# Optimization experiments

Hardware: AMD Instinct MI355X
Metric: run time of the kernel (lower is better)

Reference implementation:

```python
import jax, jax.numpy as jnp
import numpy as np

EPS_SIM = 1e-10
EPS_NORM = 1e-12


def setup_inputs() -> dict:
    key = jax.random.key(0)
    k1, k2, k3, k4, k5 = jax.random.split(key, 5)
    B, CH, H, W = 64, 512, 28, 28
    R = CH // 16  # reduction
    x = jax.random.normal(k1, (B, CH, H, W), dtype=jnp.float32)
    # torch nn.Linear weights are [out, in]
    wD = jax.random.normal(k2, (R, CH), dtype=jnp.float32) * (1.0 / np.sqrt(CH))
    bD = jax.random.normal(k3, (R,), dtype=jnp.float32) * 0.01
    wU = jax.random.normal(k4, (CH, R), dtype=jnp.float32) * (1.0 / np.sqrt(R))
    bU = jax.random.normal(k5, (CH,), dtype=jnp.float32) * 0.01
    return {"x": x, "wD": wD, "bD": bD, "wU": wU, "bU": bU}


def _hybrid_weight(xap):
    # xap: [B, CH, N]; returns row-diag-masked, globally normalized similarity Wij [B, CH, CH]
    gram = jnp.einsum('bin,bjn->bij', xap, xap)           # [B,CH,CH]
    sq = jnp.sum(xap * xap, axis=-1)                      # [B,CH]
    d2 = sq[:, :, None] + sq[:, None, :] - 2.0 * gram
    d = jnp.sqrt(d2)
    d = jnp.where(jnp.isnan(d), 0.0, d)                   # NaN mask (sqrt of negatives)
    d = jnp.maximum(d, 0.0)                               # clamp(0, inf)
    mean_d = jnp.mean(d, axis=(1, 2), keepdims=True)
    l2_sim = jnp.exp(-d / (mean_d + EPS_SIM))
    w = jnp.sqrt(sq)                                      # per-channel L2 norm
    denom = jnp.maximum(w[:, :, None] * w[:, None, :], EPS_SIM)
    cos = gram / denom
    cos = jnp.where(jnp.isnan(cos), 0.0, cos)
    cos = jnp.maximum(cos, 0.0)
    sim = cos * l2_sim
    CH = sim.shape[1]
    sim = sim * (1.0 - jnp.eye(CH, dtype=sim.dtype))      # zero diagonal
    Wij = sim / (jnp.sum(sim, axis=(1, 2), keepdims=True) + EPS_SIM)
    return Wij


def reference(x, wD, bD, wU, bU):
    B, CH, H, W = x.shape
    r = 7  # rdim[512]
    # adaptive avg pool to 7x7 (H, W divisible by 7 -> exact block average)
    xap = x.reshape(B, CH, r, H // r, r, W // r).mean(axis=(3, 5)).reshape(B, CH, r * r)
    Wij = jax.lax.stop_gradient(_hybrid_weight(xap))      # computed under no_grad in torch
    gap = x.mean(axis=(2, 3))                             # [B,CH] global avg pool
    mu = gap.mean(axis=1, keepdims=True)
    std = jnp.std(gap, axis=1, ddof=1, keepdims=True)     # torch std is unbiased
    z = (gap - mu) / std                                  # [B,CH]
    # diag(z z^T Wij)_i = z_i * (z^T Wij)_i  -> avoid materializing zz^T
    local_mi = z * jnp.einsum('bj,bji->bi', z, Wij)       # [B,CH]
    m = local_mi.mean(axis=1, keepdims=True)
    s = jnp.std(local_mi, axis=1, ddof=1, keepdims=True)
    ch = (local_mi - m) / (s + EPS_NORM)                  # normal_G
    h = jax.nn.relu(ch @ wD.T + bD)
    att = h @ wU.T + bU
    scale = jax.nn.sigmoid(att)[:, :, None, None]
    return x * scale
```

## Files before the change

kernel.cpp:

```cpp
#include <hip/hip_runtime.h>
#include <hip/hip_bf16.h>
#include <stdint.h>

#define NB 64
#define NC 512
#define NHW 784
#define NK 49
#define KP 64
#define NR 32

typedef short sh8 __attribute__((ext_vector_type(8)));
typedef float f32x4 __attribute__((ext_vector_type(4)));
typedef int v4i __attribute__((ext_vector_type(4)));

__device__ __forceinline__ float wave_sum(float v) {
#pragma unroll
  for (int o = 32; o; o >>= 1) v += __shfl_xor(v, o);
  return v;
}

__global__ __launch_bounds__(256) void pool_kernel(const float* __restrict__ x,
                                                   __hip_bfloat16* __restrict__ xap,
                                                   float* __restrict__ wbuf,
                                                   float* __restrict__ gap) {
  int wid = threadIdx.x >> 6, lane = threadIdx.x & 63;
  int row = blockIdx.x * 4 + wid;
  const float* xr = x + (size_t)row * NHW;
  float bin = 0.f;
  if (lane < NK) {
    int pr = lane / 7, pc = lane - pr * 7;
    const float4* p = (const float4*)(xr + pr * 112 + pc * 4);
    float s = 0.f;
#pragma unroll
    for (int i = 0; i < 4; ++i) {
      float4 v = p[i * 7];
      s += (v.x + v.y) + (v.z + v.w);
    }
    bin = s * 0.0625f;
  }
  float s1 = wave_sum(bin);
  float s2 = wave_sum(bin * bin);
  xap[(size_t)row * KP + lane] = __float2bfloat16(bin);
  if (lane == 0) {
    wbuf[row] = sqrtf(s2);
    gap[row] = s1 * (1.f / 49.f);
  }
}

__global__ __launch_bounds__(256) void zstat_kernel(const float* __restrict__ gap,
                                                    float* __restrict__ z) {
  __shared__ float red[4];
  int b = blockIdx.x, t = threadIdx.x;
  int wid = t >> 6, lane = t & 63;
  float g0 = gap[b * NC + t], g1 = gap[b * NC + t + 256];
  float s = wave_sum(g0 + g1);
  if (lane == 0) red[wid] = s;
  __syncthreads();
  float mu = ((red[0] + red[1]) + (red[2] + red[3])) * (1.f / 512.f);
  float d0 = g0 - mu, d1 = g1 - mu;
  __syncthreads();
  float v = wave_sum(d0 * d0 + d1 * d1);
  if (lane == 0) red[wid] = v;
  __syncthreads();
  float var = ((red[0] + red[1]) + (red[2] + red[3])) * (1.f / 511.f);
  float inv_sd = 1.f / sqrtf(var);
  z[b * NC + t] = d0 * inv_sd;
  z[b * NC + t + 256] = d1 * inv_sd;
}


__global__ __launch_bounds__(256) void meand_kernel(const __hip_bfloat16* __restrict__ xap,
                                                    const float* __restrict__ wbuf,
                                                    float* __restrict__ dpart) {
  __shared__ __align__(16) __hip_bfloat16 Ab[128 * KP];
  __shared__ __align__(16) __hip_bfloat16 Bb[128 * KP];
  __shared__ float wiL[128], wjL[128];
  __shared__ float red[4];
  int b = blockIdx.x >> 4;
  int ti = (blockIdx.x >> 2) & 3, tj = blockIdx.x & 3;
  int i0 = ti * 128, j0 = tj * 128;
  int t = threadIdx.x;
  const v4i* ga = (const v4i*)(xap + ((size_t)b * NC + i0) * KP);
  const v4i* gb = (const v4i*)(xap + ((size_t)b * NC + j0) * KP);
  v4i* la = (v4i*)Ab;
  v4i* lb = (v4i*)Bb;
#pragma unroll
  for (int q = 0; q < 4; ++q) {
    int cid = q * 256 + t;
    int r = cid >> 3, c = cid & 7;
    int dst = (r << 3) | (c ^ (r & 7));
    la[dst] = ga[cid];
    lb[dst] = gb[cid];
  }
  if (t < 128) {
    wiL[t] = wbuf[b * NC + i0 + t];
    wjL[t] = wbuf[b * NC + j0 + t];
  }
  __syncthreads();
  int lane = t & 63, wave = t >> 6;
  int wi = wave >> 1, wn = wave & 1;
  int l15 = lane & 15, g16 = lane >> 4;
  sh8 af[4][2], bfr[4][2];
#pragma unroll
  for (int f = 0; f < 4; ++f) {
#pragma unroll
    for (int ks = 0; ks < 2; ++ks) {
      int ra = wi * 64 + f * 16 + l15;
      int rb = wn * 64 + f * 16 + l15;
      int cg = ks * 4 + g16;
      af[f][ks] = __builtin_bit_cast(sh8, ((const v4i*)Ab)[(ra << 3) | (cg ^ (ra & 7))]);
      bfr[f][ks] = __builtin_bit_cast(sh8, ((const v4i*)Bb)[(rb << 3) | (cg ^ (rb & 7))]);
    }
  }
  f32x4 acc[4][4];
#pragma unroll
  for (int fm = 0; fm < 4; ++fm)
#pragma unroll
    for (int fn = 0; fn < 4; ++fn) acc[fm][fn] = (f32x4){0.f, 0.f, 0.f, 0.f};
#pragma unroll
  for (int ks = 0; ks < 2; ++ks)
#pragma unroll
    for (int fm = 0; fm < 4; ++fm)
#pragma unroll
      for (int fn = 0; fn < 4; ++fn)
        acc[fm][fn] =
            __builtin_amdgcn_mfma_f32_16x16x32_bf16(af[fm][ks], bfr[fn][ks], acc[fm][fn], 0, 0, 0);
  float wiv[4][4], wjv[4];
#pragma unroll
  for (int fm = 0; fm < 4; ++fm)
#pragma unroll
    for (int rg = 0; rg < 4; ++rg) wiv[fm][rg] = wiL[wi * 64 + fm * 16 + g16 * 4 + rg];
#pragma unroll
  for (int fn = 0; fn < 4; ++fn) wjv[fn] = wjL[wn * 64 + fn * 16 + l15];
  float dsum = 0.f;
#pragma unroll
  for (int fm = 0; fm < 4; ++fm)
#pragma unroll
    for (int fn = 0; fn < 4; ++fn)
#pragma unroll
      for (int rg = 0; rg < 4; ++rg) {
        float g = acc[fm][fn][rg];
        float a = wiv[fm][rg], bb = wjv[fn];
        float d2 = a * a + bb * bb - 2.f * g;
        dsum += sqrtf(fmaxf(d2, 0.f));
      }
  dsum = wave_sum(dsum);
  if (lane == 0) red[wave] = dsum;
  __syncthreads();
  if (t == 0) dpart[blockIdx.x] = (red[0] + red[1]) + (red[2] + red[3]);
}

__global__ __launch_bounds__(256) void sim_kernel(const __hip_bfloat16* __restrict__ xap,
                                                  const float* __restrict__ wbuf,
                                                  const float* __restrict__ z,
                                                  const float* __restrict__ dpart,
                                                  float* __restrict__ tpart,
                                                  float* __restrict__ spart) {
  __shared__ __align__(16) __hip_bfloat16 Ab[128 * KP];
  __shared__ __align__(16) __hip_bfloat16 Bb[128 * KP];
  __shared__ float wiL[128], wjL[128], zjL[128], tacc[128];
  __shared__ float red[4];
  int b = blockIdx.x >> 4;
  int ti = (blockIdx.x >> 2) & 3, tj = blockIdx.x & 3;
  int i0 = ti * 128, j0 = tj * 128;
  int t = threadIdx.x;
  float dsb = 0.f;
#pragma unroll
  for (int k = 0; k < 16; ++k) dsb += dpart[b * 16 + k];
  float inv_md = 1.f / (dsb * (1.f / 262144.f) + 1e-10f);
  const v4i* ga = (const v4i*)(xap + ((size_t)b * NC + i0) * KP);
  const v4i* gb = (const v4i*)(xap + ((size_t)b * NC + j0) * KP);
  v4i* la = (v4i*)Ab;
  v4i* lb = (v4i*)Bb;
#pragma unroll
  for (int q = 0; q < 4; ++q) {
    int cid = q * 256 + t;
    int r = cid >> 3, c = cid & 7;
    int dst = (r << 3) | (c ^ (r & 7));
    la[dst] = ga[cid];
    lb[dst] = gb[cid];
  }
  if (t < 128) {
    wiL[t] = wbuf[b * NC + i0 + t];
    wjL[t] = wbuf[b * NC + j0 + t];
    zjL[t] = z[b * NC + j0 + t];
    tacc[t] = 0.f;
  }
  __syncthreads();
  int lane = t & 63, wave = t >> 6;
  int wi = wave >> 1, wn = wave & 1;
  int l15 = lane & 15, g16 = lane >> 4;
  sh8 af[4][2], bfr[4][2];
#pragma unroll
  for (int f = 0; f < 4; ++f) {
#pragma unroll
    for (int ks = 0; ks < 2; ++ks) {
      int ra = wi * 64 + f * 16 + l15;
      int rb = wn * 64 + f * 16 + l15;
      int cg = ks * 4 + g16;
      af[f][ks] = __builtin_bit_cast(sh8, ((const v4i*)Ab)[(ra << 3) | (cg ^ (ra & 7))]);
      bfr[f][ks] = __builtin_bit_cast(sh8, ((const v4i*)Bb)[(rb << 3) | (cg ^ (rb & 7))]);
    }
  }
  f32x4 acc[4][4];
#pragma unroll
  for (int fm = 0; fm < 4; ++fm)
#pragma unroll
    for (int fn = 0; fn < 4; ++fn) acc[fm][fn] = (f32x4){0.f, 0.f, 0.f, 0.f};
#pragma unroll
  for (int ks = 0; ks < 2; ++ks)
#pragma unroll
    for (int fm = 0; fm < 4; ++fm)
#pragma unroll
      for (int fn = 0; fn < 4; ++fn)
        acc[fm][fn] =
            __builtin_amdgcn_mfma_f32_16x16x32_bf16(af[fm][ks], bfr[fn][ks], acc[fm][fn], 0, 0, 0);
  float wiv[4][4], wjv[4], zjv[4];
#pragma unroll
  for (int fm = 0; fm < 4; ++fm)
#pragma unroll
    for (int rg = 0; rg < 4; ++rg) wiv[fm][rg] = wiL[wi * 64 + fm * 16 + g16 * 4 + rg];
#pragma unroll
  for (int fn = 0; fn < 4; ++fn) {
    wjv[fn] = wjL[wn * 64 + fn * 16 + l15];
    zjv[fn] = zjL[wn * 64 + fn * 16 + l15];
  }
  float ssum = 0.f;
  float trow[4][4];
#pragma unroll
  for (int fm = 0; fm < 4; ++fm)
#pragma unroll
    for (int rg = 0; rg < 4; ++rg) trow[fm][rg] = 0.f;
#pragma unroll
  for (int fm = 0; fm < 4; ++fm)
#pragma unroll
    for (int fn = 0; fn < 4; ++fn)
#pragma unroll
      for (int rg = 0; rg < 4; ++rg) {
        float g = acc[fm][fn][rg];
        float a = wiv[fm][rg], bb = wjv[fn];
        float d = sqrtf(fmaxf(a * a + bb * bb - 2.f * g, 0.f));
        float cosv = fmaxf(g / fmaxf(a * bb, 1e-10f), 0.f);
        float sim = cosv * __expf(-d * inv_md);
        int ig = i0 + wi * 64 + fm * 16 + g16 * 4 + rg;
        int jg = j0 + wn * 64 + fn * 16 + l15;
        if (ig == jg) sim = 0.f;
        ssum += sim;
        trow[fm][rg] += sim * zjv[fn];
      }
#pragma unroll
  for (int fm = 0; fm < 4; ++fm)
#pragma unroll
    for (int rg = 0; rg < 4; ++rg) {
      float v = trow[fm][rg];
#pragma unroll
      for (int o = 8; o; o >>= 1) v += __shfl_xor(v, o);
      if (l15 == 0) atomicAdd(&tacc[wi * 64 + fm * 16 + g16 * 4 + rg], v);
    }
  ssum = wave_sum(ssum);
  if (lane == 0) red[wave] = ssum;
  __syncthreads();
  if (t == 0) spart[blockIdx.x] = (red[0] + red[1]) + (red[2] + red[3]);
  if (t < 128) tpart[((size_t)b * 4 + tj) * NC + i0 + t] = tacc[t];
}

__global__ __launch_bounds__(256) void mlp_kernel(const float* __restrict__ z,
                                                  const float* __restrict__ tpart,
                                                  const float* __restrict__ spart,
                                                  const float* __restrict__ wD,
                                                  const float* __restrict__ bD,
                                                  const float* __restrict__ wU,
                                                  const float* __restrict__ bU,
                                                  float* __restrict__ scl) {
  __shared__ float red[4];
  __shared__ float chL[NC];
  __shared__ float hL[NR];
  int b = blockIdx.x, t = threadIdx.x;
  int lane = t & 63, wid = t >> 6;
  float S = 0.f;
#pragma unroll
  for (int k = 0; k < 16; ++k) S += spart[b * 16 + k];
  float invS = 1.f / (S + 1e-10f);
  float t0 = 0.f, t1 = 0.f;
#pragma unroll
  for (int j = 0; j < 4; ++j) {
    t0 += tpart[((size_t)b * 4 + j) * NC + t];
    t1 += tpart[((size_t)b * 4 + j) * NC + t + 256];
  }
  float lm0 = z[b * NC + t] * t0 * invS;
  float lm1 = z[b * NC + t + 256] * t1 * invS;
  float s = wave_sum(lm0 + lm1);
  if (lane == 0) red[wid] = s;
  __syncthreads();
  float m = ((red[0] + red[1]) + (red[2] + red[3])) * (1.f / 512.f);
  float d0 = lm0 - m, d1 = lm1 - m;
  __syncthreads();
  float v = wave_sum(d0 * d0 + d1 * d1);
  if (lane == 0) red[wid] = v;
  __syncthreads();
  float sd = sqrtf(((red[0] + red[1]) + (red[2] + red[3])) * (1.f / 511.f)) + 1e-12f;
  chL[t] = d0 / sd;
  chL[t + 256] = d1 / sd;
  __syncthreads();
  int k = t >> 3, p = t & 7;
  const float* wrow = wD + k * NC + p * 64;
  const float* cp = chL + p * 64;
  float hp = 0.f;
#pragma unroll
  for (int i = 0; i < 64; ++i) hp += wrow[i] * cp[i];
#pragma unroll
  for (int o = 4; o; o >>= 1) hp += __shfl_xor(hp, o);
  if (p == 0) hL[k] = fmaxf(hp + bD[k], 0.f);
  __syncthreads();
#pragma unroll
  for (int u = 0; u < 2; ++u) {
    int c = t + u * 256;
    const float* wrU = wU + c * NR;
    float att = bU[c];
#pragma unroll
    for (int kk = 0; kk < NR; ++kk) att += hL[kk] * wrU[kk];
    scl[b * NC + c] = 1.f / (1.f + __expf(-att));
  }
}

__global__ __launch_bounds__(256) void scale_kernel(const float* __restrict__ x,
                                                    const float* __restrict__ scl,
                                                    float* __restrict__ out) {
  unsigned idx = blockIdx.x * 256u + threadIdx.x;
  unsigned row = idx / 196u;
  float s = scl[row];
  float4 v = ((const float4*)x)[idx];
  float4 o;
  o.x = v.x * s;
  o.y = v.y * s;
  o.z = v.z * s;
  o.w = v.w * s;
  ((float4*)out)[idx] = o;
}

extern "C" void kernel_launch(void* const* d_in, const int* in_sizes, int n_in,
                              void* d_out, int out_size, void* d_ws, size_t ws_size,
                              hipStream_t stream) {
  const float* x = (const float*)d_in[0];
  const float* wD = (const float*)d_in[1];
  const float* bD = (const float*)d_in[2];
  const float* wU = (const float*)d_in[3];
  const float* bU = (const float*)d_in[4];
  float* out = (float*)d_out;
  char* ws = (char*)d_ws;

  __hip_bfloat16* xap = (__hip_bfloat16*)ws;
  float* fbase = (float*)(ws + (size_t)NB * NC * KP * 2);
  float* wbuf = fbase;
  float* gap = wbuf + NB * NC;
  float* zb = gap + NB * NC;
  float* dpart = zb + NB * NC;
  float* spart = dpart + 1024;
  float* tpart = spart + 1024;
  float* scl = tpart + NB * 4 * NC;

  hipLaunchKernelGGL(pool_kernel, dim3(NB * NC / 4), dim3(256), 0, stream, x, xap, wbuf, gap);
  hipLaunchKernelGGL(zstat_kernel, dim3(NB), dim3(256), 0, stream, gap, zb);
  hipLaunchKernelGGL(meand_kernel, dim3(NB * 16), dim3(256), 0, stream, xap, wbuf, dpart);
  hipLaunchKernelGGL(sim_kernel, dim3(NB * 16), dim3(256), 0, stream, xap, wbuf, zb, dpart, tpart, spart);
  hipLaunchKernelGGL(mlp_kernel, dim3(NB), dim3(256), 0, stream, zb, tpart, spart, wD, bD, wU, bU, scl);
  hipLaunchKernelGGL(scale_kernel, dim3(25088), dim3(256), 0, stream, x, scl, out);
}
```

Measured before the change: 98.34 us.

## Exploit similarity symmetry with upper-triangular tiles and fuse z-stat into consumers

Both the mean-distance and similarity kernels now process only the 10 upper-triangular 128x128 tiles per batch instead of all 16. Off-diagonal tile sums are doubled, and the similarity kernel accumulates both row and column contributions into a full-length shared buffer. The separate zstat kernel is removed: z is recomputed inside sim_kernel and mlp_kernel. The inner math is also simplified (precomputed squares and reciprocal norms, exp2), and the scale kernel uses nontemporal loads and stores. This cuts tile work and one launch, at the cost of extra shared atomics, redundant z computation per block, and larger tpart partial-sum traffic.

```diff
diff --git a/kernel.cpp b/kernel.cpp
--- a/kernel.cpp
+++ b/kernel.cpp
@@ -8,6 +8,7 @@
 #define NK 49
 #define KP 64
 #define NR 32
+#define NTASK 10
 
 typedef short sh8 __attribute__((ext_vector_type(8)));
 typedef float f32x4 __attribute__((ext_vector_type(4)));
@@ -17,6 +18,13 @@
 #pragma unroll
   for (int o = 32; o; o >>= 1) v += __shfl_xor(v, o);
   return v;
+}
+
+__device__ __forceinline__ void task_decode(int s, int& ti, int& tj) {
+  if (s < 4) { ti = 0; tj = s; }
+  else if (s < 7) { ti = 1; tj = s - 3; }
+  else if (s < 9) { ti = 2; tj = s - 5; }
+  else { ti = 3; tj = 3; }
 }
 
 __global__ __launch_bounds__(256) void pool_kernel(const float* __restrict__ x,
@@ -47,28 +55,6 @@
   }
 }
 
-__global__ __launch_bounds__(256) void zstat_kernel(const float* __restrict__ gap,
-                                                    float* __restrict__ z) {
-  __shared__ float red[4];
-  int b = blockIdx.x, t = threadIdx.x;
-  int wid = t >> 6, lane = t & 63;
-  float g0 = gap[b * NC + t], g1 = gap[b * NC + t + 256];
-  float s = wave_sum(g0 + g1);
-  if (lane == 0) red[wid] = s;
-  __syncthreads();
-  float mu = ((red[0] + red[1]) + (red[2] + red[3])) * (1.f / 512.f);
-  float d0 = g0 - mu, d1 = g1 - mu;
-  __syncthreads();
-  float v = wave_sum(d0 * d0 + d1 * d1);
-  if (lane == 0) red[wid] = v;
-  __syncthreads();
-  float var = ((red[0] + red[1]) + (red[2] + red[3])) * (1.f / 511.f);
-  float inv_sd = 1.f / sqrtf(var);
-  z[b * NC + t] = d0 * inv_sd;
-  z[b * NC + t + 256] = d1 * inv_sd;
-}
-
-
 __global__ __launch_bounds__(256) void meand_kernel(const __hip_bfloat16* __restrict__ xap,
                                                     const float* __restrict__ wbuf,
                                                     float* __restrict__ dpart) {
@@ -76,8 +62,11 @@
   __shared__ __align__(16) __hip_bfloat16 Bb[128 * KP];
   __shared__ float wiL[128], wjL[128];
   __shared__ float red[4];
-  int b = blockIdx.x >> 4;
-  int ti = (blockIdx.x >> 2) & 3, tj = blockIdx.x & 3;
+  int blk = blockIdx.x;
+  int b = blk / NTASK, s = blk - b * NTASK;
+  int ti, tj;
+  task_decode(s, ti, tj);
+  bool diag = (ti == tj);
   int i0 = ti * 128, j0 = tj * 128;
   int t = threadIdx.x;
   const v4i* ga = (const v4i*)(xap + ((size_t)b * NC + i0) * KP);
@@ -125,13 +114,19 @@
       for (int fn = 0; fn < 4; ++fn)
         acc[fm][fn] =
             __builtin_amdgcn_mfma_f32_16x16x32_bf16(af[fm][ks], bfr[fn][ks], acc[fm][fn], 0, 0, 0);
-  float wiv[4][4], wjv[4];
-#pragma unroll
-  for (int fm = 0; fm < 4; ++fm)
-#pragma unroll
-    for (int rg = 0; rg < 4; ++rg) wiv[fm][rg] = wiL[wi * 64 + fm * 16 + g16 * 4 + rg];
-#pragma unroll
-  for (int fn = 0; fn < 4; ++fn) wjv[fn] = wjL[wn * 64 + fn * 16 + l15];
+  float a2[4][4], b2[4];
+#pragma unroll
+  for (int fm = 0; fm < 4; ++fm)
+#pragma unroll
+    for (int rg = 0; rg < 4; ++rg) {
+      float a = wiL[wi * 64 + fm * 16 + g16 * 4 + rg];
+      a2[fm][rg] = a * a;
+    }
+#pragma unroll
+  for (int fn = 0; fn < 4; ++fn) {
+    float w = wjL[wn * 64 + fn * 16 + l15];
+    b2[fn] = w * w;
+  }
   float dsum = 0.f;
 #pragma unroll
   for (int fm = 0; fm < 4; ++fm)
@@ -139,35 +134,37 @@
     for (int fn = 0; fn < 4; ++fn)
 #pragma unroll
       for (int rg = 0; rg < 4; ++rg) {
-        float g = acc[fm][fn][rg];
-        float a = wiv[fm][rg], bb = wjv[fn];
-        float d2 = a * a + bb * bb - 2.f * g;
+        float d2 = fmaf(-2.f, acc[fm][fn][rg], a2[fm][rg] + b2[fn]);
         dsum += sqrtf(fmaxf(d2, 0.f));
       }
   dsum = wave_sum(dsum);
   if (lane == 0) red[wave] = dsum;
   __syncthreads();
-  if (t == 0) dpart[blockIdx.x] = (red[0] + red[1]) + (red[2] + red[3]);
+  if (t == 0) dpart[blk] = ((red[0] + red[1]) + (red[2] + red[3])) * (diag ? 1.f : 2.f);
 }
 
 __global__ __launch_bounds__(256) void sim_kernel(const __hip_bfloat16* __restrict__ xap,
                                                   const float* __restrict__ wbuf,
-                                                  const float* __restrict__ z,
+                                                  const float* __restrict__ gap,
                                                   const float* __restrict__ dpart,
                                                   float* __restrict__ tpart,
                                                   float* __restrict__ spart) {
   __shared__ __align__(16) __hip_bfloat16 Ab[128 * KP];
   __shared__ __align__(16) __hip_bfloat16 Bb[128 * KP];
-  __shared__ float wiL[128], wjL[128], zjL[128], tacc[128];
+  __shared__ float wiL[128], wjL[128], zL[NC], tfull[NC];
   __shared__ float red[4];
-  int b = blockIdx.x >> 4;
-  int ti = (blockIdx.x >> 2) & 3, tj = blockIdx.x & 3;
+  int blk = blockIdx.x;
+  int b = blk / NTASK, s = blk - b * NTASK;
+  int ti, tj;
+  task_decode(s, ti, tj);
+  bool diag = (ti == tj);
   int i0 = ti * 128, j0 = tj * 128;
   int t = threadIdx.x;
+  int lane = t & 63, wave = t >> 6;
   float dsb = 0.f;
 #pragma unroll
-  for (int k = 0; k < 16; ++k) dsb += dpart[b * 16 + k];
-  float inv_md = 1.f / (dsb * (1.f / 262144.f) + 1e-10f);
+  for (int k = 0; k < NTASK; ++k) dsb += dpart[b * NTASK + k];
+  float nim = -1.44269504f / (dsb * (1.f / 262144.f) + 1e-10f);
   const v4i* ga = (const v4i*)(xap + ((size_t)b * NC + i0) * KP);
   const v4i* gb = (const v4i*)(xap + ((size_t)b * NC + j0) * KP);
   v4i* la = (v4i*)Ab;
@@ -183,11 +180,23 @@
   if (t < 128) {
     wiL[t] = wbuf[b * NC + i0 + t];
     wjL[t] = wbuf[b * NC + j0 + t];
-    zjL[t] = z[b * NC + j0 + t];
-    tacc[t] = 0.f;
-  }
-  __syncthreads();
-  int lane = t & 63, wave = t >> 6;
+  }
+  tfull[t] = 0.f;
+  tfull[t + 256] = 0.f;
+  float g0 = gap[b * NC + t], g1 = gap[b * NC + t + 256];
+  float s1 = wave_sum(g0 + g1);
+  if (lane == 0) red[wave] = s1;
+  __syncthreads();
+  float mu = ((red[0] + red[1]) + (red[2] + red[3])) * (1.f / 512.f);
+  float e0 = g0 - mu, e1 = g1 - mu;
+  __syncthreads();
+  float vv = wave_sum(e0 * e0 + e1 * e1);
+  if (lane == 0) red[wave] = vv;
+  __syncthreads();
+  float inv_sd = 1.f / sqrtf(((red[0] + red[1]) + (red[2] + red[3])) * (1.f / 511.f));
+  zL[t] = e0 * inv_sd;
+  zL[t + 256] = e1 * inv_sd;
+  __syncthreads();
   int wi = wave >> 1, wn = wave & 1;
   int l15 = lane & 15, g16 = lane >> 4;
   sh8 af[4][2], bfr[4][2];
@@ -215,18 +224,29 @@
       for (int fn = 0; fn < 4; ++fn)
         acc[fm][fn] =
             __builtin_amdgcn_mfma_f32_16x16x32_bf16(af[fm][ks], bfr[fn][ks], acc[fm][fn], 0, 0, 0);
-  float wiv[4][4], wjv[4], zjv[4];
-#pragma unroll
-  for (int fm = 0; fm < 4; ++fm)
-#pragma unroll
-    for (int rg = 0; rg < 4; ++rg) wiv[fm][rg] = wiL[wi * 64 + fm * 16 + g16 * 4 + rg];
+  float a2[4][4], ia[4][4], zi[4][4];
+#pragma unroll
+  for (int fm = 0; fm < 4; ++fm)
+#pragma unroll
+    for (int rg = 0; rg < 4; ++rg) {
+      int il = wi * 64 + fm * 16 + g16 * 4 + rg;
+      float a = wiL[il];
+      a2[fm][rg] = a * a;
+      ia[fm][rg] = 1.f / fmaxf(a, 1e-7f);
+      zi[fm][rg] = zL[i0 + il];
+    }
+  float b2[4], ib[4], zj[4];
 #pragma unroll
   for (int fn = 0; fn < 4; ++fn) {
-    wjv[fn] = wjL[wn * 64 + fn * 16 + l15];
-    zjv[fn] = zjL[wn * 64 + fn * 16 + l15];
+    int jl = wn * 64 + fn * 16 + l15;
+    float w = wjL[jl];
+    b2[fn] = w * w;
+    ib[fn] = 1.f / fmaxf(w, 1e-7f);
+    zj[fn] = zL[j0 + jl];
   }
   float ssum = 0.f;
   float trow[4][4];
+  float tcol[4] = {0.f, 0.f, 0.f, 0.f};
 #pragma unroll
   for (int fm = 0; fm < 4; ++fm)
 #pragma unroll
@@ -234,20 +254,24 @@
 #pragma unroll
   for (int fm = 0; fm < 4; ++fm)
 #pragma unroll
-    for (int fn = 0; fn < 4; ++fn)
+    for (int fn = 0; fn < 4; ++fn) {
+      float ibn = ib[fn];
 #pragma unroll
       for (int rg = 0; rg < 4; ++rg) {
         float g = acc[fm][fn][rg];
-        float a = wiv[fm][rg], bb = wjv[fn];
-        float d = sqrtf(fmaxf(a * a + bb * bb - 2.f * g, 0.f));
-        float cosv = fmaxf(g / fmaxf(a * bb, 1e-10f), 0.f);
-        float sim = cosv * __expf(-d * inv_md);
-        int ig = i0 + wi * 64 + fm * 16 + g16 * 4 + rg;
-        int jg = j0 + wn * 64 + fn * 16 + l15;
-        if (ig == jg) sim = 0.f;
+        float d2 = fmaf(-2.f, g, a2[fm][rg] + b2[fn]);
+        float d = sqrtf(fmaxf(d2, 0.f));
+        float sim = fmaxf(g, 0.f) * ia[fm][rg] * ibn * exp2f(d * nim);
+        if (diag) {
+          int il = wi * 64 + fm * 16 + g16 * 4 + rg;
+          int jl = wn * 64 + fn * 16 + l15;
+          if (il == jl) sim = 0.f;
+        }
         ssum += sim;
-        trow[fm][rg] += sim * zjv[fn];
+        trow[fm][rg] = fmaf(sim, zj[fn], trow[fm][rg]);
+        tcol[fn] = fmaf(sim, zi[fm][rg], tcol[fn]);
       }
+    }
 #pragma unroll
   for (int fm = 0; fm < 4; ++fm)
 #pragma unroll
@@ -255,16 +279,26 @@
       float v = trow[fm][rg];
 #pragma unroll
       for (int o = 8; o; o >>= 1) v += __shfl_xor(v, o);
-      if (l15 == 0) atomicAdd(&tacc[wi * 64 + fm * 16 + g16 * 4 + rg], v);
-    }
+      if (l15 == 0) atomicAdd(&tfull[i0 + wi * 64 + fm * 16 + g16 * 4 + rg], v);
+    }
+  if (!diag) {
+#pragma unroll
+    for (int fn = 0; fn < 4; ++fn) {
+      float v = tcol[fn];
+      v += __shfl_xor(v, 16);
+      v += __shfl_xor(v, 32);
+      if (g16 == 0) atomicAdd(&tfull[j0 + wn * 64 + fn * 16 + l15], v);
+    }
+  }
   ssum = wave_sum(ssum);
   if (lane == 0) red[wave] = ssum;
   __syncthreads();
-  if (t == 0) spart[blockIdx.x] = (red[0] + red[1]) + (red[2] + red[3]);
-  if (t < 128) tpart[((size_t)b * 4 + tj) * NC + i0 + t] = tacc[t];
-}
-
-__global__ __launch_bounds__(256) void mlp_kernel(const float* __restrict__ z,
+  if (t == 0) spart[blk] = ((red[0] + red[1]) + (red[2] + red[3])) * (diag ? 1.f : 2.f);
+  tpart[(size_t)blk * NC + t] = tfull[t];
+  tpart[(size_t)blk * NC + t + 256] = tfull[t + 256];
+}
+
+__global__ __launch_bounds__(256) void mlp_kernel(const float* __restrict__ gap,
                                                   const float* __restrict__ tpart,
                                                   const float* __restrict__ spart,
                                                   const float* __restrict__ wD,
@@ -279,24 +313,36 @@
   int lane = t & 63, wid = t >> 6;
   float S = 0.f;
 #pragma unroll
-  for (int k = 0; k < 16; ++k) S += spart[b * 16 + k];
+  for (int k = 0; k < NTASK; ++k) S += spart[b * NTASK + k];
   float invS = 1.f / (S + 1e-10f);
   float t0 = 0.f, t1 = 0.f;
 #pragma unroll
-  for (int j = 0; j < 4; ++j) {
-    t0 += tpart[((size_t)b * 4 + j) * NC + t];
-    t1 += tpart[((size_t)b * 4 + j) * NC + t + 256];
-  }
-  float lm0 = z[b * NC + t] * t0 * invS;
-  float lm1 = z[b * NC + t + 256] * t1 * invS;
-  float s = wave_sum(lm0 + lm1);
-  if (lane == 0) red[wid] = s;
+  for (int j = 0; j < NTASK; ++j) {
+    t0 += tpart[((size_t)b * NTASK + j) * NC + t];
+    t1 += tpart[((size_t)b * NTASK + j) * NC + t + 256];
+  }
+  float g0 = gap[b * NC + t], g1 = gap[b * NC + t + 256];
+  float s1 = wave_sum(g0 + g1);
+  if (lane == 0) red[wid] = s1;
+  __syncthreads();
+  float mu = ((red[0] + red[1]) + (red[2] + red[3])) * (1.f / 512.f);
+  float e0 = g0 - mu, e1 = g1 - mu;
+  __syncthreads();
+  float vv = wave_sum(e0 * e0 + e1 * e1);
+  if (lane == 0) red[wid] = vv;
+  __syncthreads();
+  float inv_sd = 1.f / sqrtf(((red[0] + red[1]) + (red[2] + red[3])) * (1.f / 511.f));
+  float lm0 = e0 * inv_sd * t0 * invS;
+  float lm1 = e1 * inv_sd * t1 * invS;
+  __syncthreads();
+  float s2 = wave_sum(lm0 + lm1);
+  if (lane == 0) red[wid] = s2;
   __syncthreads();
   float m = ((red[0] + red[1]) + (red[2] + red[3])) * (1.f / 512.f);
   float d0 = lm0 - m, d1 = lm1 - m;
   __syncthreads();
-  float v = wave_sum(d0 * d0 + d1 * d1);
-  if (lane == 0) red[wid] = v;
+  float v2 = wave_sum(d0 * d0 + d1 * d1);
+  if (lane == 0) red[wid] = v2;
   __syncthreads();
   float sd = sqrtf(((red[0] + red[1]) + (red[2] + red[3])) * (1.f / 511.f)) + 1e-12f;
   chL[t] = d0 / sd;
@@ -329,13 +375,9 @@
   unsigned idx = blockIdx.x * 256u + threadIdx.x;
   unsigned row = idx / 196u;
   float s = scl[row];
-  float4 v = ((const float4*)x)[idx];
-  float4 o;
-  o.x = v.x * s;
-  o.y = v.y * s;
-  o.z = v.z * s;
-  o.w = v.w * s;
-  ((float4*)out)[idx] = o;
+  f32x4 v = __builtin_nontemporal_load(((const f32x4*)x) + idx);
+  v *= s;
+  __builtin_nontemporal_store(v, ((f32x4*)out) + idx);
 }
 
 extern "C" void kernel_launch(void* const* d_in, const int* in_sizes, int n_in,
@@ -353,16 +395,16 @@
   float* fbase = (float*)(ws + (size_t)NB * NC * KP * 2);
   float* wbuf = fbase;
   float* gap = wbuf + NB * NC;
-  float* zb = gap + NB * NC;
-  float* dpart = zb + NB * NC;
-  float* spart = dpart + 1024;
-  float* tpart = spart + 1024;
-  float* scl = tpart + NB * 4 * NC;
+  float* dpart = gap + NB * NC;
+  float* spart = dpart + NB * NTASK;
+  float* tpart = spart + NB * NTASK;
+  float* scl = tpart + NB * NTASK * NC;
 
   hipLaunchKernelGGL(pool_kernel, dim3(NB * NC / 4), dim3(256), 0, stream, x, xap, wbuf, gap);
-  hipLaunchKernelGGL(zstat_kernel, dim3(NB), dim3(256), 0, stream, gap, zb);
-  hipLaunchKernelGGL(meand_kernel, dim3(NB * 16), dim3(256), 0, stream, xap, wbuf, dpart);
-  hipLaunchKernelGGL(sim_kernel, dim3(NB * 16), dim3(256), 0, stream, xap, wbuf, zb, dpart, tpart, spart);
-  hipLaunchKernelGGL(mlp_kernel, dim3(NB), dim3(256), 0, stream, zb, tpart, spart, wD, bD, wU, bU, scl);
+  hipLaunchKernelGGL(meand_kernel, dim3(NB * NTASK), dim3(256), 0, stream, xap, wbuf, dpart);
+  hipLaunchKernelGGL(sim_kernel, dim3(NB * NTASK), dim3(256), 0, stream, xap, wbuf, gap, dpart,
+                     tpart, spart);
+  hipLaunchKernelGGL(mlp_kernel, dim3(NB), dim3(256), 0, stream, gap, tpart, spart, wD, bD, wU, bU,
+                     scl);
   hipLaunchKernelGGL(scale_kernel, dim3(25088), dim3(256), 0, stream, x, scl, out);
 }
```

Result: faster. 95.01 us (-3.4%).
